# Optimization experiments

Hardware: AMD Instinct MI355X
Metric: run time of the kernel (lower is better)

The kernel has to match this reference:

```python
import jax, jax.numpy as jnp
import numpy as np

HIDDEN = 1024
HEADS = 16
KNN = 20
EDGE_DICT = 64


def setup_inputs() -> dict:
    key = jax.random.key(0)
    ks = jax.random.split(key, 16)
    B, S, L = 2, 2000, 100
    w = lambda k, shp: jax.random.normal(k, shp, dtype=jnp.float32) * 0.02
    return {
        "c_mask": jax.random.randint(ks[0], (L,), 0, 2),
        "degrees_vec": jax.random.randint(ks[1], (L,), 0, EDGE_DICT),
        "q": jax.random.normal(ks[2], (B, S, HIDDEN), dtype=jnp.float32),
        "k": jax.random.normal(ks[3], (B, S, HIDDEN), dtype=jnp.float32),
        "v": jax.random.normal(ks[4], (B, S, HIDDEN), dtype=jnp.float32),
        "Wq": w(ks[5], (HIDDEN, HIDDEN)), "bq": jnp.zeros((HIDDEN,), jnp.float32),
        "Wk": w(ks[6], (HIDDEN, HIDDEN)), "bk": jnp.zeros((HIDDEN,), jnp.float32),
        "Wv": w(ks[7], (HIDDEN, HIDDEN)), "bv": jnp.zeros((HIDDEN,), jnp.float32),
        "Wo": w(ks[8], (HIDDEN, HIDDEN)), "bo": jnp.zeros((HIDDEN,), jnp.float32),
        "edge_emb": w(ks[9], (EDGE_DICT, HIDDEN)),
        "mask_emb": w(ks[10], (2, HIDDEN)),
    }


def reference(c_mask, degrees_vec, q, k, v, Wq, bq, Wk, bk, Wv, bv, Wo, bo, edge_emb, mask_emb):
    B, S, _ = q.shape
    d = HIDDEN // HEADS
    scale = d ** -0.5
    # torch Linear: x @ W.T + b
    qh = (q @ Wq.T + bq).reshape(B, S, HEADS, d)
    kh = (k @ Wk.T + bk).reshape(B, S, HEADS, d)
    vh = (v @ Wv.T + bv).reshape(B, S, HEADS, d)
    scores = jnp.einsum("bqhd,bkhd->bhqk", qh * scale, kh)  # [B,H,S,S]
    # edge bias: outer product of repeated embedding lookups -> [S,S]
    de = edge_emb[jnp.repeat(degrees_vec, KNN)]  # [S, hidden]
    ce = mask_emb[jnp.repeat(c_mask, KNN)]       # [S, hidden]
    bias = de @ ce.T                              # [S, S]
    attn = jax.nn.softmax(scores + bias[None, None], axis=-1)
    out = jnp.einsum("bhqk,bkhd->bqhd", attn, vh).reshape(B, S, HIDDEN)
    return out @ Wo.T + bo
```

## Files before the change

### kernel.cpp

```cpp
#include <hip/hip_runtime.h>
#include <cstdint>
#include <cstddef>

#define HIDDEN 1024
#define HEADS  16
#define DHEAD  64
#define BB     2
#define SS     2000
#define KNNR   20
#define MM     (BB*SS)

typedef __attribute__((ext_vector_type(8)))  short short8;
typedef __attribute__((ext_vector_type(4)))  float f32x4;
typedef __attribute__((ext_vector_type(16))) float f32x16;
typedef unsigned short ushort_t;
typedef unsigned int   uint_t;

__device__ __forceinline__ ushort_t f2bf(float f) {
    union { float f; uint_t u; } v; v.f = f;
    uint_t r = (v.u + 0x7FFFu + ((v.u >> 16) & 1u)) >> 16;
    return (ushort_t)r;
}
__device__ __forceinline__ float bf2f(ushort_t b) {
    union { uint_t u; float f; } v; v.u = ((uint_t)b) << 16;
    return v.f;
}

__global__ void cvt3_kernel(const float* __restrict__ a, const float* __restrict__ b,
                            const float* __restrict__ c,
                            ushort_t* __restrict__ oa, ushort_t* __restrict__ ob,
                            ushort_t* __restrict__ oc, int n)
{
    const float* src; ushort_t* dst;
    if (blockIdx.y == 0)      { src = a; dst = oa; }
    else if (blockIdx.y == 1) { src = b; dst = ob; }
    else                      { src = c; dst = oc; }
    const int stride = gridDim.x * blockDim.x * 4;
    for (int i = (blockIdx.x * blockDim.x + threadIdx.x) * 4; i < n; i += stride) {
        float4 v = *(const float4*)(src + i);
        ushort_t o[4] = { f2bf(v.x), f2bf(v.y), f2bf(v.z), f2bf(v.w) };
        *(uint2*)(dst + i) = *(uint2*)o;
    }
}

__global__ void cvt4_kernel(const float* __restrict__ a, const float* __restrict__ b,
                            const float* __restrict__ c, const float* __restrict__ d,
                            ushort_t* __restrict__ oa, ushort_t* __restrict__ ob,
                            ushort_t* __restrict__ oc, ushort_t* __restrict__ od, int n)
{
    const float* src; ushort_t* dst;
    if (blockIdx.y == 0)      { src = a; dst = oa; }
    else if (blockIdx.y == 1) { src = b; dst = ob; }
    else if (blockIdx.y == 2) { src = c; dst = oc; }
    else                      { src = d; dst = od; }
    const int stride = gridDim.x * blockDim.x * 4;
    for (int i = (blockIdx.x * blockDim.x + threadIdx.x) * 4; i < n; i += stride) {
        float4 v = *(const float4*)(src + i);
        ushort_t o[4] = { f2bf(v.x), f2bf(v.y), f2bf(v.z), f2bf(v.w) };
        *(uint2*)(dst + i) = *(uint2*)o;
    }
}

__global__ void bias_table_kernel(const float* __restrict__ edge_emb,
                                  const float* __restrict__ mask_emb,
                                  float* __restrict__ P)
{
    const int e = blockIdx.x >> 1;
    const int m = blockIdx.x & 1;
    const int lane = threadIdx.x;
    const float* er = edge_emb + (size_t)e * HIDDEN;
    const float* mr = mask_emb + (size_t)m * HIDDEN;
    float s = 0.f;
    for (int d = lane; d < HIDDEN; d += 64) s += er[d] * mr[d];
    #pragma unroll
    for (int off = 32; off > 0; off >>= 1) s += __shfl_down(s, off, 64);
    if (lane == 0) P[e * 2 + m] = s;
}

template<int OUT_BF16>
__global__ __launch_bounds__(256, 2)
void gemm_bf16(const ushort_t* __restrict__ A, const ushort_t* __restrict__ Bw,
               const float* __restrict__ bias, void* __restrict__ Cp, int M)
{
    __shared__ __align__(16) ushort_t As[128 * 32];
    __shared__ __align__(16) ushort_t Bs[128 * 32];
    const int t = threadIdx.x, l = t & 63, w = t >> 6;
    const int wr = w >> 1, wc = w & 1;
    const int g = l >> 4, r16 = l & 15;
    const int m0 = blockIdx.y * 128, n0 = blockIdx.x * 128;

    f32x4 acc[4][4];
    #pragma unroll
    for (int i = 0; i < 4; ++i)
        #pragma unroll
        for (int j = 0; j < 4; ++j)
            #pragma unroll
            for (int r = 0; r < 4; ++r) acc[i][j][r] = 0.f;

    for (int k0 = 0; k0 < 1024; k0 += 32) {
        __syncthreads();
        #pragma unroll
        for (int i = 0; i < 2; ++i) {
            const int c = i * 256 + w * 64 + l;
            const int row = c >> 2, kc = c & 3;
            int ra = m0 + row; ra = ra < M ? ra : M - 1;
            const ushort_t* srcA = A + (size_t)ra * 1024 + k0 + kc * 8;
            const ushort_t* srcB = Bw + (size_t)(n0 + row) * 1024 + k0 + kc * 8;
            __builtin_amdgcn_global_load_lds(
                (const __attribute__((address_space(1))) void*)srcA,
                (__attribute__((address_space(3))) void*)&As[(i * 256 + w * 64) * 8],
                16, 0, 0);
            __builtin_amdgcn_global_load_lds(
                (const __attribute__((address_space(1))) void*)srcB,
                (__attribute__((address_space(3))) void*)&Bs[(i * 256 + w * 64) * 8],
                16, 0, 0);
        }
        __syncthreads();

        short8 af[4], bf_[4];
        #pragma unroll
        for (int m = 0; m < 4; ++m)
            af[m] = *(const short8*)&As[(wr * 64 + m * 16 + r16) * 32 + g * 8];
        #pragma unroll
        for (int n = 0; n < 4; ++n)
            bf_[n] = *(const short8*)&Bs[(wc * 64 + n * 16 + r16) * 32 + g * 8];
        #pragma unroll
        for (int m = 0; m < 4; ++m)
            #pragma unroll
            for (int n = 0; n < 4; ++n)
                acc[m][n] = __builtin_amdgcn_mfma_f32_16x16x32_bf16(af[m], bf_[n], acc[m][n], 0, 0, 0);
    }

    float bv[4];
    #pragma unroll
    for (int n = 0; n < 4; ++n) bv[n] = bias[n0 + wc * 64 + n * 16 + r16];

    #pragma unroll
    for (int m = 0; m < 4; ++m)
        #pragma unroll
        for (int n = 0; n < 4; ++n)
            #pragma unroll
            for (int r = 0; r < 4; ++r) {
                const int row = m0 + wr * 64 + m * 16 + g * 4 + r;
                const int col = n0 + wc * 64 + n * 16 + r16;
                if (row < M) {
                    const float v = acc[m][n][r] + bv[n];
                    if (OUT_BF16) ((ushort_t*)Cp)[(size_t)row * 1024 + col] = f2bf(v);
                    else          ((float*)Cp)[(size_t)row * 1024 + col] = v;
                }
            }
}

__global__ __launch_bounds__(256)
void transpose_v(const ushort_t* __restrict__ vh, ushort_t* __restrict__ vhT)
{
    __shared__ __align__(16) ushort_t T[64 * 72];
    const int bh = blockIdx.y, b = bh >> 4, h = bh & 15;
    const int s0 = blockIdx.x * 64;
    const int t = threadIdx.x;
    #pragma unroll
    for (int i = 0; i < 2; ++i) {
        const int c = 2 * t + i, srow = c >> 3, d8 = c & 7;
        const int s = s0 + srow;
        uint4 val = make_uint4(0, 0, 0, 0);
        if (s < SS) val = *(const uint4*)(vh + (size_t)(b * SS + s) * 1024 + h * 64 + d8 * 8);
        *(uint4*)&T[srow * 72 + d8 * 8] = val;
    }
    __syncthreads();
    #pragma unroll
    for (int i = 0; i < 2; ++i) {
        const int c = 2 * t + i, drow = c >> 3, s8 = c & 7;
        ushort_t tmp[8];
        #pragma unroll
        for (int j = 0; j < 8; ++j) tmp[j] = T[(s8 * 8 + j) * 72 + drow];
        *(uint4*)(vhT + (size_t)(bh * 64 + drow) * 2048 + s0 + s8 * 8) = *(uint4*)tmp;
    }
}

__global__ __launch_bounds__(256, 2)
void attn_mfma(const ushort_t* __restrict__ qh, const ushort_t* __restrict__ kh,
               const ushort_t* __restrict__ vhT, ushort_t* __restrict__ ctx,
               const int* __restrict__ c_mask, const int* __restrict__ degrees,
               const float* __restrict__ P)
{
    __shared__ __align__(16) ushort_t Ks[64 * 72];
    __shared__ __align__(16) ushort_t Vt[64 * 72];
    __shared__ __align__(16) ushort_t Ps[4][32 * 72];
    __shared__ int cm[100];

    const int t = threadIdx.x, l = t & 63, w = t >> 6;
    const int lo = l & 31, hi = l >> 5;
    const int bh = blockIdx.y, b = bh >> 4, h = bh & 15;
    const int qw = blockIdx.x * 128 + w * 32;

    if (t < 100) cm[t] = c_mask[t];

    short8 qf[4];
    {
        int qr = qw + lo; qr = qr < SS ? qr : SS - 1;
        const ushort_t* qp = qh + (size_t)(b * SS + qr) * 1024 + h * 64 + hi * 8;
        #pragma unroll
        for (int ks = 0; ks < 4; ++ks) qf[ks] = *(const short8*)(qp + ks * 16);
    }

    float db[16], denom[16];
    #pragma unroll
    for (int r = 0; r < 16; ++r) {
        const int rp = (r & 3) + 8 * (r >> 2) + 4 * hi;
        int qr = qw + rp; qr = qr < SS ? qr : SS - 1;
        const int dv = degrees[qr / KNNR];
        db[r] = P[dv * 2 + 1] - P[dv * 2 + 0];
        denom[r] = 0.f;
    }

    f32x16 accO[2];
    #pragma unroll
    for (int n = 0; n < 2; ++n)
        #pragma unroll
        for (int i = 0; i < 16; ++i) accO[n][i] = 0.f;

    uint4 kreg[2], vreg[2];
    {
        #pragma unroll
        for (int i = 0; i < 2; ++i) {
            const int c = 2 * t + i, row = c >> 3, e8 = c & 7;
            int s = row; s = s < SS ? s : SS - 1;
            kreg[i] = *(const uint4*)(kh + (size_t)(b * SS + s) * 1024 + h * 64 + e8 * 8);
            vreg[i] = *(const uint4*)(vhT + (size_t)(bh * 64 + row) * 2048 + e8 * 8);
        }
    }

    for (int kt = 0; kt < 32; ++kt) {
        const int kt0 = kt * 64;
        __syncthreads();
        #pragma unroll
        for (int i = 0; i < 2; ++i) {
            const int c = 2 * t + i, row = c >> 3, e8 = c & 7;
            *(uint4*)&Ks[row * 72 + e8 * 8] = kreg[i];
            *(uint4*)&Vt[row * 72 + e8 * 8] = vreg[i];
        }
        if (kt < 31) {
            const int nt0 = kt0 + 64;
            #pragma unroll
            for (int i = 0; i < 2; ++i) {
                const int c = 2 * t + i, row = c >> 3, e8 = c & 7;
                int s = nt0 + row; s = s < SS ? s : SS - 1;
                kreg[i] = *(const uint4*)(kh + (size_t)(b * SS + s) * 1024 + h * 64 + e8 * 8);
                vreg[i] = *(const uint4*)(vhT + (size_t)(bh * 64 + row) * 2048 + nt0 + e8 * 8);
            }
        }
        __syncthreads();

        f32x16 sc[2];
        #pragma unroll
        for (int n = 0; n < 2; ++n)
            #pragma unroll
            for (int i = 0; i < 16; ++i) sc[n][i] = 0.f;
        #pragma unroll
        for (int ks = 0; ks < 4; ++ks)
            #pragma unroll
            for (int n = 0; n < 2; ++n) {
                const short8 kf = *(const short8*)&Ks[(n * 32 + lo) * 72 + ks * 16 + hi * 8];
                sc[n] = __builtin_amdgcn_mfma_f32_32x32x16_bf16(qf[ks], kf, sc[n], 0, 0, 0);
            }

        int kb[2];
        #pragma unroll
        for (int n = 0; n < 2; ++n) {
            int col = kt0 + n * 32 + lo; col = col < SS ? col : SS - 1;
            kb[n] = cm[col / KNNR];
        }
        #pragma unroll
        for (int n = 0; n < 2; ++n)
            #pragma unroll
            for (int r = 0; r < 16; ++r) {
                const int rp = (r & 3) + 8 * (r >> 2) + 4 * hi;
                const float s = sc[n][r] * 0.125f + (kb[n] ? db[r] : 0.0f);
                float e = __expf(s);
                if (kt0 + n * 32 + lo >= SS) e = 0.f;
                const ushort_t pb = f2bf(e);
                denom[r] += bf2f(pb);
                Ps[w][rp * 72 + n * 32 + lo] = pb;
            }
        asm volatile("s_waitcnt lgkmcnt(0)" ::: "memory");
        __builtin_amdgcn_sched_barrier(0);

        #pragma unroll
        for (int ks = 0; ks < 4; ++ks) {
            const short8 pa = *(const short8*)&Ps[w][lo * 72 + ks * 16 + hi * 8];
            #pragma unroll
            for (int n = 0; n < 2; ++n) {
                const short8 vf = *(const short8*)&Vt[(n * 32 + lo) * 72 + ks * 16 + hi * 8];
                accO[n] = __builtin_amdgcn_mfma_f32_32x32x16_bf16(pa, vf, accO[n], 0, 0, 0);
            }
        }
    }

    #pragma unroll
    for (int r = 0; r < 16; ++r) {
        float d = denom[r];
        d += __shfl_xor(d, 1);  d += __shfl_xor(d, 2);  d += __shfl_xor(d, 4);
        d += __shfl_xor(d, 8);  d += __shfl_xor(d, 16);
        denom[r] = 1.f / d;
    }

    #pragma unroll
    for (int n = 0; n < 2; ++n)
        #pragma unroll
        for (int r = 0; r < 16; ++r) {
            const int rp = (r & 3) + 8 * (r >> 2) + 4 * hi;
            const int qr = qw + rp;
            if (qr < SS)
                ctx[(size_t)(b * SS + qr) * 1024 + h * 64 + n * 32 + lo] =
                    f2bf(accO[n][r] * denom[r]);
        }
}

extern "C" void kernel_launch(void* const* d_in, const int* in_sizes, int n_in,
                              void* d_out, int out_size, void* d_ws, size_t ws_size,
                              hipStream_t stream)
{
    const int*   c_mask   = (const int*)  d_in[0];
    const int*   degrees  = (const int*)  d_in[1];
    const float* q        = (const float*)d_in[2];
    const float* k        = (const float*)d_in[3];
    const float* v        = (const float*)d_in[4];
    const float* Wq       = (const float*)d_in[5];
    const float* bq       = (const float*)d_in[6];
    const float* Wk       = (const float*)d_in[7];
    const float* bk       = (const float*)d_in[8];
    const float* Wv       = (const float*)d_in[9];
    const float* bv       = (const float*)d_in[10];
    const float* Wo       = (const float*)d_in[11];
    const float* bo       = (const float*)d_in[12];
    const float* edge_emb = (const float*)d_in[13];
    const float* mask_emb = (const float*)d_in[14];
    float* out = (float*)d_out;

    char* ws = (char*)d_ws;
    const size_t MB = 1024 * 1024;
    ushort_t* qb   = (ushort_t*)(ws + 0 * MB);
    ushort_t* kb_  = (ushort_t*)(ws + 8 * MB);
    ushort_t* vb_  = (ushort_t*)(ws + 16 * MB);
    ushort_t* Wqb  = (ushort_t*)(ws + 24 * MB);
    ushort_t* Wkb  = (ushort_t*)(ws + 26 * MB);
    ushort_t* Wvb  = (ushort_t*)(ws + 28 * MB);
    ushort_t* Wob  = (ushort_t*)(ws + 30 * MB);
    ushort_t* qhB  = (ushort_t*)(ws + 32 * MB);
    ushort_t* khB  = (ushort_t*)(ws + 40 * MB);
    ushort_t* vhB  = (ushort_t*)(ws + 48 * MB);
    float*    P    = (float*)   (ws + 56 * MB);
    ushort_t* vhT  = kb_;
    ushort_t* ctx  = qb;

    cvt3_kernel<<<dim3(1024, 3), 256, 0, stream>>>(q, k, v, qb, kb_, vb_, MM * HIDDEN);
    cvt4_kernel<<<dim3(1024, 4), 256, 0, stream>>>(Wq, Wk, Wv, Wo, Wqb, Wkb, Wvb, Wob,
                                                   HIDDEN * HIDDEN);
    bias_table_kernel<<<dim3(128), dim3(64), 0, stream>>>(edge_emb, mask_emb, P);

    const dim3 ggrid(8, 32), gblk(256);
    gemm_bf16<1><<<ggrid, gblk, 0, stream>>>(qb,  Wqb, bq, qhB, MM);
    gemm_bf16<1><<<ggrid, gblk, 0, stream>>>(kb_, Wkb, bk, khB, MM);
    gemm_bf16<1><<<ggrid, gblk, 0, stream>>>(vb_, Wvb, bv, vhB, MM);

    transpose_v<<<dim3(32, 32), 256, 0, stream>>>(vhB, vhT);

    attn_mfma<<<dim3(16, 32), 256, 0, stream>>>(qhB, khB, vhT, ctx, c_mask, degrees, P);

    gemm_bf16<0><<<ggrid, gblk, 0, stream>>>(ctx, Wob, bo, out, MM);
}
```

Before: 336.1 us.

## Split attention and output GEMM over K with atomic reduction; fuse QKV GEMMs

The attention kernel now splits the key dimension into two halves across a third grid axis. Partial unnormalised outputs are accumulated into an fp32 buffer with atomics, partial denominators are written out, and a new divide kernel normalises and converts the result to bf16. The output projection is split-K by two with atomicAdd, the three QKV GEMMs are merged into one launch, and the softmax scale and log2e are folded into the Q projection so the kernel can use exp2f. The goal is more blocks in flight for the under-occupied attention and Wo stages, at the cost of zero-fill kernels, extra fp32 traffic, atomics and one more launch.

```diff
diff --git a/kernel.cpp b/kernel.cpp
--- a/kernel.cpp
+++ b/kernel.cpp
@@ -16,6 +16,8 @@
 typedef unsigned short ushort_t;
 typedef unsigned int   uint_t;
 
+#define LOG2E 1.4426950408889634f
+
 __device__ __forceinline__ ushort_t f2bf(float f) {
     union { float f; uint_t u; } v; v.f = f;
     uint_t r = (v.u + 0x7FFFu + ((v.u >> 16) & 1u)) >> 16;
@@ -24,6 +26,13 @@
 __device__ __forceinline__ float bf2f(ushort_t b) {
     union { uint_t u; float f; } v; v.u = ((uint_t)b) << 16;
     return v.f;
+}
+
+__global__ void zerofill_kernel(float* __restrict__ p, int n4)
+{
+    const int stride = gridDim.x * blockDim.x;
+    for (int i = blockIdx.x * blockDim.x + threadIdx.x; i < n4; i += stride)
+        *(float4*)(p + 4 * (size_t)i) = make_float4(0.f, 0.f, 0.f, 0.f);
 }
 
 __global__ void cvt3_kernel(const float* __restrict__ a, const float* __restrict__ b,
@@ -77,17 +86,16 @@
     if (lane == 0) P[e * 2 + m] = s;
 }
 
-template<int OUT_BF16>
-__global__ __launch_bounds__(256, 2)
-void gemm_bf16(const ushort_t* __restrict__ A, const ushort_t* __restrict__ Bw,
-               const float* __restrict__ bias, void* __restrict__ Cp, int M)
-{
-    __shared__ __align__(16) ushort_t As[128 * 32];
-    __shared__ __align__(16) ushort_t Bs[128 * 32];
+template<int OUT_MODE>
+__device__ __forceinline__
+void gemm_core(const ushort_t* __restrict__ A, const ushort_t* __restrict__ Bw,
+               const float* __restrict__ bias, void* __restrict__ Cp,
+               int M, int m0, int n0, int kbeg, int kend, float oscale, int addbias,
+               ushort_t* As, ushort_t* Bs)
+{
     const int t = threadIdx.x, l = t & 63, w = t >> 6;
     const int wr = w >> 1, wc = w & 1;
     const int g = l >> 4, r16 = l & 15;
-    const int m0 = blockIdx.y * 128, n0 = blockIdx.x * 128;
 
     f32x4 acc[4][4];
     #pragma unroll
@@ -97,7 +105,7 @@
             #pragma unroll
             for (int r = 0; r < 4; ++r) acc[i][j][r] = 0.f;
 
-    for (int k0 = 0; k0 < 1024; k0 += 32) {
+    for (int k0 = kbeg; k0 < kend; k0 += 32) {
         __syncthreads();
         #pragma unroll
         for (int i = 0; i < 2; ++i) {
@@ -133,7 +141,8 @@
 
     float bv[4];
     #pragma unroll
-    for (int n = 0; n < 4; ++n) bv[n] = bias[n0 + wc * 64 + n * 16 + r16];
+    for (int n = 0; n < 4; ++n)
+        bv[n] = addbias ? bias[n0 + wc * 64 + n * 16 + r16] : 0.f;
 
     #pragma unroll
     for (int m = 0; m < 4; ++m)
@@ -144,11 +153,48 @@
                 const int row = m0 + wr * 64 + m * 16 + g * 4 + r;
                 const int col = n0 + wc * 64 + n * 16 + r16;
                 if (row < M) {
-                    const float v = acc[m][n][r] + bv[n];
-                    if (OUT_BF16) ((ushort_t*)Cp)[(size_t)row * 1024 + col] = f2bf(v);
-                    else          ((float*)Cp)[(size_t)row * 1024 + col] = v;
+                    if (OUT_MODE == 1) {
+                        const float v = (acc[m][n][r] + bv[n]) * oscale;
+                        ((ushort_t*)Cp)[(size_t)row * 1024 + col] = f2bf(v);
+                    } else {
+                        atomicAdd(&((float*)Cp)[(size_t)row * 1024 + col],
+                                  acc[m][n][r] + bv[n]);
+                    }
                 }
             }
+}
+
+__global__ __launch_bounds__(256, 2)
+void qkv_gemm(const ushort_t* __restrict__ qb, const ushort_t* __restrict__ kb,
+              const ushort_t* __restrict__ vb,
+              const ushort_t* __restrict__ Wq, const ushort_t* __restrict__ Wk,
+              const ushort_t* __restrict__ Wv,
+              const float* __restrict__ bq, const float* __restrict__ bk,
+              const float* __restrict__ bv,
+              ushort_t* __restrict__ qh, ushort_t* __restrict__ kh,
+              ushort_t* __restrict__ vh)
+{
+    __shared__ __align__(16) ushort_t As[128 * 32];
+    __shared__ __align__(16) ushort_t Bs[128 * 32];
+    const int which = blockIdx.x >> 3;
+    const int n0 = (blockIdx.x & 7) * 128, m0 = blockIdx.y * 128;
+    const ushort_t* A; const ushort_t* Bw; const float* bias; ushort_t* dst;
+    float osc = 1.f;
+    if (which == 0)      { A = qb; Bw = Wq; bias = bq; dst = qh; osc = 0.125f * LOG2E; }
+    else if (which == 1) { A = kb; Bw = Wk; bias = bk; dst = kh; }
+    else                 { A = vb; Bw = Wv; bias = bv; dst = vh; }
+    gemm_core<1>(A, Bw, bias, dst, MM, m0, n0, 0, 1024, osc, 1, As, Bs);
+}
+
+__global__ __launch_bounds__(256, 2)
+void wo_gemm(const ushort_t* __restrict__ ctx, const ushort_t* __restrict__ Wo,
+             const float* __restrict__ bo, float* __restrict__ out)
+{
+    __shared__ __align__(16) ushort_t As[128 * 32];
+    __shared__ __align__(16) ushort_t Bs[128 * 32];
+    const int z = blockIdx.z;
+    gemm_core<2>(ctx, Wo, bo, out, MM, blockIdx.y * 128, blockIdx.x * 128,
+                 z * 512, z * 512 + 512, 1.f, z == 0, As, Bs);
 }
 
 __global__ __launch_bounds__(256)
@@ -179,7 +225,8 @@
 
 __global__ __launch_bounds__(256, 2)
 void attn_mfma(const ushort_t* __restrict__ qh, const ushort_t* __restrict__ kh,
-               const ushort_t* __restrict__ vhT, ushort_t* __restrict__ ctx,
+               const ushort_t* __restrict__ vhT, float* __restrict__ octx,
+               float* __restrict__ dpart,
                const int* __restrict__ c_mask, const int* __restrict__ degrees,
                const float* __restrict__ P)
 {
@@ -192,6 +239,7 @@
     const int lo = l & 31, hi = l >> 5;
     const int bh = blockIdx.y, b = bh >> 4, h = bh & 15;
     const int qw = blockIdx.x * 128 + w * 32;
+    const int z = blockIdx.z;
 
     if (t < 100) cm[t] = c_mask[t];
 
@@ -203,13 +251,13 @@
         for (int ks = 0; ks < 4; ++ks) qf[ks] = *(const short8*)(qp + ks * 16);
     }
 
-    float db[16], denom[16];
+    float db2[16], denom[16];
     #pragma unroll
     for (int r = 0; r < 16; ++r) {
         const int rp = (r & 3) + 8 * (r >> 2) + 4 * hi;
         int qr = qw + rp; qr = qr < SS ? qr : SS - 1;
         const int dv = degrees[qr / KNNR];
-        db[r] = P[dv * 2 + 1] - P[dv * 2 + 0];
+        db2[r] = (P[dv * 2 + 1] - P[dv * 2 + 0]) * LOG2E;
         denom[r] = 0.f;
     }
 
@@ -224,14 +272,14 @@
         #pragma unroll
         for (int i = 0; i < 2; ++i) {
             const int c = 2 * t + i, row = c >> 3, e8 = c & 7;
-            int s = row; s = s < SS ? s : SS - 1;
+            int s = z * 1024 + row; s = s < SS ? s : SS - 1;
             kreg[i] = *(const uint4*)(kh + (size_t)(b * SS + s) * 1024 + h * 64 + e8 * 8);
-            vreg[i] = *(const uint4*)(vhT + (size_t)(bh * 64 + row) * 2048 + e8 * 8);
-        }
-    }
-
-    for (int kt = 0; kt < 32; ++kt) {
-        const int kt0 = kt * 64;
+            vreg[i] = *(const uint4*)(vhT + (size_t)(bh * 64 + row) * 2048 + z * 1024 + e8 * 8);
+        }
+    }
+
+    for (int kt = 0; kt < 16; ++kt) {
+        const int kt0 = (z * 16 + kt) * 64;
         __syncthreads();
         #pragma unroll
         for (int i = 0; i < 2; ++i) {
@@ -239,7 +287,7 @@
             *(uint4*)&Ks[row * 72 + e8 * 8] = kreg[i];
             *(uint4*)&Vt[row * 72 + e8 * 8] = vreg[i];
         }
-        if (kt < 31) {
+        if (kt < 15) {
             const int nt0 = kt0 + 64;
             #pragma unroll
             for (int i = 0; i < 2; ++i) {
@@ -275,8 +323,8 @@
             #pragma unroll
             for (int r = 0; r < 16; ++r) {
                 const int rp = (r & 3) + 8 * (r >> 2) + 4 * hi;
-                const float s = sc[n][r] * 0.125f + (kb[n] ? db[r] : 0.0f);
-                float e = __expf(s);
+                const float s = sc[n][r] + (kb[n] ? db2[r] : 0.0f);
+                float e = exp2f(s);
                 if (kt0 + n * 32 + lo >= SS) e = 0.f;
                 const ushort_t pb = f2bf(e);
                 denom[r] += bf2f(pb);
@@ -301,7 +349,11 @@
         float d = denom[r];
         d += __shfl_xor(d, 1);  d += __shfl_xor(d, 2);  d += __shfl_xor(d, 4);
         d += __shfl_xor(d, 8);  d += __shfl_xor(d, 16);
-        denom[r] = 1.f / d;
+        if (lo == 0) {
+            const int rp = (r & 3) + 8 * (r >> 2) + 4 * hi;
+            const int qr = qw + rp;
+            if (qr < SS) dpart[(size_t)z * 32 * SS + bh * SS + qr] = d;
+        }
     }
 
     #pragma unroll
@@ -311,9 +363,25 @@
             const int rp = (r & 3) + 8 * (r >> 2) + 4 * hi;
             const int qr = qw + rp;
             if (qr < SS)
-                ctx[(size_t)(b * SS + qr) * 1024 + h * 64 + n * 32 + lo] =
-                    f2bf(accO[n][r] * denom[r]);
-        }
+                atomicAdd(&octx[(size_t)(b * SS + qr) * 1024 + h * 64 + n * 32 + lo],
+                          accO[n][r]);
+        }
+}
+
+__global__ __launch_bounds__(256)
+void divide_kernel(const float* __restrict__ octx, const float* __restrict__ dpart,
+                   ushort_t* __restrict__ ctx)
+{
+    const int i = (blockIdx.x * 256 + threadIdx.x) * 4;
+    const int row = i >> 10, col = i & 1023;
+    const int b = row >= SS ? 1 : 0;
+    const int q = row - b * SS;
+    const int h = col >> 6;
+    const size_t di = (size_t)(b * 16 + h) * SS + q;
+    const float inv = 1.f / (dpart[di] + dpart[32 * SS + di]);
+    const float4 o = *(const float4*)(octx + i);
+    ushort_t u[4] = { f2bf(o.x * inv), f2bf(o.y * inv), f2bf(o.z * inv), f2bf(o.w * inv) };
+    *(uint2*)(ctx + i) = *(uint2*)u;
 }
 
 extern "C" void kernel_launch(void* const* d_in, const int* in_sizes, int n_in,
@@ -338,34 +406,40 @@
     float* out = (float*)d_out;
 
     char* ws = (char*)d_ws;
-    const size_t MB = 1024 * 1024;
-    ushort_t* qb   = (ushort_t*)(ws + 0 * MB);
-    ushort_t* kb_  = (ushort_t*)(ws + 8 * MB);
-    ushort_t* vb_  = (ushort_t*)(ws + 16 * MB);
-    ushort_t* Wqb  = (ushort_t*)(ws + 24 * MB);
-    ushort_t* Wkb  = (ushort_t*)(ws + 26 * MB);
-    ushort_t* Wvb  = (ushort_t*)(ws + 28 * MB);
-    ushort_t* Wob  = (ushort_t*)(ws + 30 * MB);
-    ushort_t* qhB  = (ushort_t*)(ws + 32 * MB);
-    ushort_t* khB  = (ushort_t*)(ws + 40 * MB);
-    ushort_t* vhB  = (ushort_t*)(ws + 48 * MB);
-    float*    P    = (float*)   (ws + 56 * MB);
+    const size_t MiB = 1024 * 1024;
+    ushort_t* qb   = (ushort_t*)(ws + 0 * MiB);
+    ushort_t* kb_  = (ushort_t*)(ws + 8 * MiB);
+    ushort_t* vb_  = (ushort_t*)(ws + 16 * MiB);
+    ushort_t* Wqb  = (ushort_t*)(ws + 24 * MiB);
+    ushort_t* Wkb  = (ushort_t*)(ws + 26 * MiB);
+    ushort_t* Wvb  = (ushort_t*)(ws + 28 * MiB);
+    ushort_t* Wob  = (ushort_t*)(ws + 30 * MiB);
+    ushort_t* qhB  = (ushort_t*)(ws + 32 * MiB);
+    ushort_t* khB  = (ushort_t*)(ws + 40 * MiB);
+    ushort_t* vhB  = (ushort_t*)(ws + 48 * MiB);
+    float*    octx = (float*)   (ws + 56 * MiB);
+    float*    dpart= (float*)   (ws + 56 * MiB + 16384000);
+    float*    P    = (float*)   (ws + 73 * MiB);
     ushort_t* vhT  = kb_;
     ushort_t* ctx  = qb;
+
+    zerofill_kernel<<<2048, 256, 0, stream>>>(octx, (16384000 + 512000) / 16);
+    zerofill_kernel<<<2048, 256, 0, stream>>>(out, MM * HIDDEN / 4);
 
     cvt3_kernel<<<dim3(1024, 3), 256, 0, stream>>>(q, k, v, qb, kb_, vb_, MM * HIDDEN);
     cvt4_kernel<<<dim3(1024, 4), 256, 0, stream>>>(Wq, Wk, Wv, Wo, Wqb, Wkb, Wvb, Wob,
                                                    HIDDEN * HIDDEN);
     bias_table_kernel<<<dim3(128), dim3(64), 0, stream>>>(edge_emb, mask_emb, P);
 
-    const dim3 ggrid(8, 32), gblk(256);
-    gemm_bf16<1><<<ggrid, gblk, 0, stream>>>(qb,  Wqb, bq, qhB, MM);
-    gemm_bf16<1><<<ggrid, gblk, 0, stream>>>(kb_, Wkb, bk, khB, MM);
-    gemm_bf16<1><<<ggrid, gblk, 0, stream>>>(vb_, Wvb, bv, vhB, MM);
+    qkv_gemm<<<dim3(24, 32), 256, 0, stream>>>(qb, kb_, vb_, Wqb, Wkb, Wvb,
+                                               bq, bk, bv, qhB, khB, vhB);
 
     transpose_v<<<dim3(32, 32), 256, 0, stream>>>(vhB, vhT);
 
-    attn_mfma<<<dim3(16, 32), 256, 0, stream>>>(qhB, khB, vhT, ctx, c_mask, degrees, P);
-
-    gemm_bf16<0><<<ggrid, gblk, 0, stream>>>(ctx, Wob, bo, out, MM);
-}
+    attn_mfma<<<dim3(16, 32, 2), 256, 0, stream>>>(qhB, khB, vhT, octx, dpart,
+                                                   c_mask, degrees, P);
+
+    divide_kernel<<<4000, 256, 0, stream>>>(octx, dpart, ctx);
+
+    wo_gemm<<<dim3(8, 32, 2), 256, 0, stream>>>(ctx, Wob, bo, out);
+}
```

Result: slower. 384.8 us (+14.5%).
